# Performance work log

Hardware: AMD Instinct MI355X
Metric: run time of the kernel (lower is better)

The kernel has to match this reference:

```python
import jax, jax.numpy as jnp
import numpy as np

B, S, D, H = 2, 2048, 1024, 16
DH = D // H

def setup_inputs() -> dict:
    key = jax.random.key(0)
    ks = jax.random.split(key, 9)
    s = 1.0 / np.sqrt(D)
    def lin(k):
        kw, kb = jax.random.split(k)
        W = jax.random.uniform(kw, (D, D), jnp.float32, -s, s)
        b = jax.random.uniform(kb, (D,), jnp.float32, -s, s)
        return W, b
    Wq, bq = lin(ks[0]); Wk, bk = lin(ks[1]); Wv, bv = lin(ks[2]); Wo, bo = lin(ks[3])
    x = jax.random.normal(ks[4], (B, S, D), jnp.float32)
    return {"x": x, "Wq": Wq, "bq": bq, "Wk": Wk, "bk": bk,
            "Wv": Wv, "bv": bv, "Wo": Wo, "bo": bo}

def _split_heads(t):
    # [B,S,D] -> [B,H,S,DH]
    return t.reshape(B, S, H, DH).transpose(0, 2, 1, 3)

def reference(x, Wq, bq, Wk, bk, Wv, bv, Wo, bo):
    # torch Linear: y = x @ W.T + b
    q = _split_heads(x @ Wq.T + bq)
    k = _split_heads(x @ Wk.T + bk)
    v = _split_heads(x @ Wv.T + bv)
    scores = jnp.einsum('bhqd,bhkd->bhqk', q, k) / jnp.sqrt(jnp.float32(DH))
    p = jax.nn.softmax(scores, axis=-1)  # dropout is identity in eval
    o = jnp.einsum('bhqk,bhkd->bhqd', p, v)
    o = o.transpose(0, 2, 1, 3).reshape(B, S, D)  # combine heads
    return o @ Wo.T + bo
```

## Files before the change

### kernel.cpp

```cpp
#include <hip/hip_runtime.h>


typedef __bf16 bf16;
typedef bf16 bf16x8 __attribute__((ext_vector_type(8)));
typedef bf16 bf16x4 __attribute__((ext_vector_type(4)));
typedef short s16x4 __attribute__((ext_vector_type(4)));
typedef float f32x4 __attribute__((ext_vector_type(4)));

#define MFMA32(a, b, c) __builtin_amdgcn_mfma_f32_16x16x32_bf16(a, b, c, 0, 0, 0)

#if __has_builtin(__builtin_amdgcn_mfma_f32_16x16x16bf16_1k)
#define HAVE_MFMA16 1
#define MFMA16(a, b, c) __builtin_amdgcn_mfma_f32_16x16x16bf16_1k(a, b, c, 0, 0, 0)
#else
#define HAVE_MFMA16 0
#endif

#define GLL(g, l) __builtin_amdgcn_global_load_lds(                              \
    (const __attribute__((address_space(1))) void*)(const void*)(g),             \
    (__attribute__((address_space(3))) void*)(void*)(l), 16, 0, 0)

union pk4 { bf16x4 h; s16x4 s; unsigned int d[2]; };

__global__ __launch_bounds__(256)
void cvt_bf16(const float* __restrict__ x,  const float* __restrict__ Wq,
              const float* __restrict__ Wk, const float* __restrict__ Wv,
              const float* __restrict__ Wo,
              bf16* __restrict__ xb, bf16* __restrict__ wqb, bf16* __restrict__ wkb,
              bf16* __restrict__ wvb, bf16* __restrict__ wob)
{
    const int idx = blockIdx.x * 256 + threadIdx.x;
    const float* src; bf16* dst; int off;
    if (idx < 1048576) { src = x; dst = xb; off = idx; }
    else {
        const int r = idx - 1048576;
        const int seg = r >> 18;
        off = r & 262143;
        src = (seg == 0) ? Wq : (seg == 1) ? Wk : (seg == 2) ? Wv : Wo;
        dst = (seg == 0) ? wqb : (seg == 1) ? wkb : (seg == 2) ? wvb : wob;
    }
    const float4 v = ((const float4*)src)[off];
    bf16x4 o = {(bf16)v.x, (bf16)v.y, (bf16)v.z, (bf16)v.w};
    *(bf16x4*)(dst + (size_t)off * 4) = o;
}

__global__ __launch_bounds__(256)
void qkv_gemm(const bf16* __restrict__ xb,
              const bf16* __restrict__ wqb, const float* __restrict__ bq,
              const bf16* __restrict__ wkb, const float* __restrict__ bk,
              const bf16* __restrict__ wvb, const float* __restrict__ bv,
              bf16* __restrict__ q_ws, bf16* __restrict__ k_ws, bf16* __restrict__ v_ws)
{
    const int z = blockIdx.z;
    const bf16*  W    = (z == 0) ? wqb : (z == 1) ? wkb : wvb;
    const float* bias = (z == 0) ? bq  : (z == 1) ? bk  : bv;

    __shared__ bf16 As[128][32];
    __shared__ bf16 Bs[128][32];
    __shared__ bf16 Vt[64][132];

    const int m0 = blockIdx.x * 128;
    const int n0 = blockIdx.y * 128;
    const int t    = threadIdx.x;
    const int wave = t >> 6;
    const int lane = t & 63;
    const int lr   = lane & 15;
    const int quad = lane >> 4;
    const int wm = (wave & 1) * 64;
    const int wn = (wave >> 1) * 64;

    const int srow = wave * 32 + (lane >> 2);
    const int scol = (lane & 3) * 8;
    const bf16* ga0 = xb + (size_t)(m0 + srow) * 1024 + scol;
    const bf16* ga1 = xb + (size_t)(m0 + srow + 16) * 1024 + scol;
    const bf16* gb0 = W  + (size_t)(n0 + srow) * 1024 + scol;
    const bf16* gb1 = W  + (size_t)(n0 + srow + 16) * 1024 + scol;
    bf16* la0 = &As[srow][scol];
    bf16* la1 = &As[srow + 16][scol];
    bf16* lb0 = &Bs[srow][scol];
    bf16* lb1 = &Bs[srow + 16][scol];

    f32x4 acc[4][4] = {};

    for (int k0 = 0; k0 < 1024; k0 += 32) {
        GLL(ga0 + k0, la0);
        GLL(ga1 + k0, la1);
        GLL(gb0 + k0, lb0);
        GLL(gb1 + k0, lb1);
        __syncthreads();

        bf16x8 af[4], bfr[4];
        #pragma unroll
        for (int i = 0; i < 4; i++) af[i]  = *(const bf16x8*)&As[wm + i*16 + lr][quad*8];
        #pragma unroll
        for (int j = 0; j < 4; j++) bfr[j] = *(const bf16x8*)&Bs[wn + j*16 + lr][quad*8];
        #pragma unroll
        for (int i = 0; i < 4; i++)
            #pragma unroll
            for (int j = 0; j < 4; j++)
                acc[i][j] = MFMA32(af[i], bfr[j], acc[i][j]);
        __syncthreads();
    }

    if (z < 2) {
        bf16* dstb = (z == 0) ? q_ws : k_ws;
        const float sc = (z == 0) ? 0.125f : 1.0f;
        #pragma unroll
        for (int j = 0; j < 4; j++) {
            const int col = n0 + wn + j * 16 + lr;
            const float bb = bias[col];
            const int h  = col >> 6;
            const int dh = col & 63;
            #pragma unroll
            for (int i = 0; i < 4; i++)
                #pragma unroll
                for (int r = 0; r < 4; r++) {
                    const int row = m0 + wm + i * 16 + quad * 4 + r;
                    const int bi = row >> 11, si = row & 2047;
                    dstb[(((size_t)bi * 16 + h) * 2048 + si) * 64 + dh] =
                        (bf16)((acc[i][j][r] + bb) * sc);
                }
        }
    } else {
        const int bi = m0 >> 11, si0 = m0 & 2047;
        #pragma unroll
        for (int ph = 0; ph < 2; ph++) {
            if ((wave >> 1) == ph) {
                #pragma unroll
                for (int j = 0; j < 4; j++) {
                    const float bb = bias[n0 + ph * 64 + j * 16 + lr];
                    #pragma unroll
                    for (int i = 0; i < 4; i++)
                        #pragma unroll
                        for (int r = 0; r < 4; r++)
                            Vt[j * 16 + lr][wm + i * 16 + quad * 4 + r] =
                                (bf16)(acc[i][j][r] + bb);
                }
            }
            __syncthreads();
            const int c  = t >> 2;
            const int sc_ = (t & 3) * 32;
            const int col = n0 + ph * 64 + c;
            const int h = col >> 6, dh = col & 63;
            bf16* dst = v_ws + (((size_t)bi * 16 + h) * 64 + dh) * 2048 + si0 + sc_;
            #pragma unroll
            for (int e = 0; e < 4; e++)
                *(bf16x8*)(dst + e * 8) = *(const bf16x8*)&Vt[c][sc_ + e * 8];
            __syncthreads();
        }
    }
}

__global__ __launch_bounds__(256, 4)
void attn(const bf16* __restrict__ q_ws, const bf16* __restrict__ k_ws,
          const bf16* __restrict__ v_ws, bf16* __restrict__ o_ws)
{
    const int qt = blockIdx.x;
    const int bh = blockIdx.y;
    const int b_ = bh >> 4, h = bh & 15;

    const bf16* qbase = q_ws + (size_t)bh * 2048 * 64;
    const bf16* kbase = k_ws + (size_t)bh * 2048 * 64;
    const bf16* vbase = v_ws + (size_t)bh * 64 * 2048;

    __shared__ bf16 Ks[128][72];
    __shared__ bf16 Vs[64][136];

    const int t    = threadIdx.x;
    const int wave = t >> 6;
    const int lane = t & 63;
    const int lr   = lane & 15;
    const int quad = lane >> 4;

    bf16x8 aq[2];
    #pragma unroll
    for (int kc = 0; kc < 2; kc++)
        aq[kc] = *(const bf16x8*)(qbase +
            (size_t)(qt*64 + wave*16 + lr) * 64 + kc*32 + quad*8);

    float m_i = -1e30f, l_i = 0.f;
    f32x4 o_accT[4] = {};
    const float C = 1.44269504f;

    for (int kt = 0; kt < 16; kt++) {
        __syncthreads();
        #pragma unroll
        for (int u = 0; u < 4; u++) {
            const int c = t + u * 256;
            *(bf16x8*)&Ks[c >> 3][(c & 7) * 8] =
                *(const bf16x8*)(kbase + (size_t)kt * 128 * 64 + c * 8);
            const int d = c >> 4, off = (c & 15) * 8;
            *(bf16x8*)&Vs[d][off] =
                *(const bf16x8*)(vbase + (size_t)d * 2048 + kt*128 + off);
        }
        __syncthreads();

        f32x4 sacc[8];
        #pragma unroll
        for (int j = 0; j < 8; j++) {
            bf16x8 kf0 = *(const bf16x8*)&Ks[j*16 + lr][quad*8];
            bf16x8 kf1 = *(const bf16x8*)&Ks[j*16 + lr][32 + quad*8];
            f32x4 a = {0.f, 0.f, 0.f, 0.f};
            a = MFMA32(kf0, aq[0], a);
            a = MFMA32(kf1, aq[1], a);
            sacc[j] = a;
        }

        float m = -1e30f;
        #pragma unroll
        for (int j = 0; j < 8; j++)
            #pragma unroll
            for (int r = 0; r < 4; r++) m = fmaxf(m, sacc[j][r]);
        m = fmaxf(m, __shfl_xor(m, 16));
        m = fmaxf(m, __shfl_xor(m, 32));
        const float nm = fmaxf(m_i, m);
        const float al = exp2f((m_i - nm) * C);
        m_i = nm;
        const float nmc = nm * C;
        float rs = 0.f;
        #pragma unroll
        for (int j = 0; j < 8; j++)
            #pragma unroll
            for (int r = 0; r < 4; r++) {
                const float p = exp2f(fmaf(sacc[j][r], C, -nmc));
                sacc[j][r] = p;
                rs += p;
            }
        #pragma unroll
        for (int n = 0; n < 4; n++)
            #pragma unroll
            for (int r = 0; r < 4; r++) o_accT[n][r] *= al;
        rs += __shfl_xor(rs, 16);
        rs += __shfl_xor(rs, 32);
        l_i = l_i * al + rs;

#if HAVE_MFMA16
        #pragma unroll
        for (int j = 0; j < 8; j++) {
            pk4 pf;
            pf.h = bf16x4{(bf16)sacc[j][0], (bf16)sacc[j][1],
                          (bf16)sacc[j][2], (bf16)sacc[j][3]};
            #pragma unroll
            for (int fb = 0; fb < 4; fb++) {
                pk4 vf;
                *(unsigned long long*)vf.d =
                    *(const unsigned long long*)&Vs[fb*16 + lr][j*16 + quad*4];
                o_accT[fb] = MFMA16(vf.s, pf.s, o_accT[fb]);
            }
        }
#else
        unsigned int p0[8], p1[8];
        #pragma unroll
        for (int j = 0; j < 8; j++) {
            pk4 pf;
            pf.h = bf16x4{(bf16)sacc[j][0], (bf16)sacc[j][1],
                          (bf16)sacc[j][2], (bf16)sacc[j][3]};
            p0[j] = pf.d[0]; p1[j] = pf.d[1];
        }
        const int srcA = lr + 16 * ((2 * quad) & 3);
        const int srcB = lr + 16 * ((2 * quad + 1) & 3);
        const bool hi = (quad >> 1) != 0;
        #pragma unroll
        for (int c = 0; c < 4; c++) {
            unsigned int a0 = __shfl(p0[2*c], srcA), a1 = __shfl(p0[2*c+1], srcA);
            unsigned int b0 = __shfl(p1[2*c], srcA), b1 = __shfl(p1[2*c+1], srcA);
            unsigned int c0 = __shfl(p0[2*c], srcB), c1 = __shfl(p0[2*c+1], srcB);
            unsigned int d0 = __shfl(p1[2*c], srcB), d1 = __shfl(p1[2*c+1], srcB);
            unsigned int fr[4];
            fr[0] = hi ? a1 : a0;
            fr[1] = hi ? b1 : b0;
            fr[2] = hi ? c1 : c0;
            fr[3] = hi ? d1 : d0;
            bf16x8 pf8 = *(bf16x8*)fr;
            #pragma unroll
            for (int fb = 0; fb < 4; fb++) {
                bf16x8 vf8 = *(const bf16x8*)&Vs[fb*16 + lr][c*32 + quad*8];
                o_accT[fb] = MFMA32(vf8, pf8, o_accT[fb]);
            }
        }
#endif
    }

    const float inv = 1.0f / l_i;
    const int s = qt*64 + wave*16 + lr;
    #pragma unroll
    for (int fb = 0; fb < 4; fb++) {
        bf16x4 ov = {(bf16)(o_accT[fb][0] * inv), (bf16)(o_accT[fb][1] * inv),
                     (bf16)(o_accT[fb][2] * inv), (bf16)(o_accT[fb][3] * inv)};
        *(bf16x4*)(o_ws + ((size_t)b_ * 2048 + s) * 1024 + h*64 + fb*16 + quad*4) = ov;
    }
}

__global__ __launch_bounds__(256)
void out_gemm(const bf16* __restrict__ o_ws,
              const bf16* __restrict__ wob, const float* __restrict__ bo,
              float* __restrict__ out)
{
    __shared__ bf16 As[128][32];
    __shared__ bf16 Bs[128][32];

    const int m0 = blockIdx.x * 128;
    const int n0 = blockIdx.y * 128;
    const int t    = threadIdx.x;
    const int wave = t >> 6;
    const int lane = t & 63;
    const int lr   = lane & 15;
    const int quad = lane >> 4;
    const int wm = (wave & 1) * 64;
    const int wn = (wave >> 1) * 64;

    const int srow = wave * 32 + (lane >> 2);
    const int scol = (lane & 3) * 8;
    const bf16* ga0 = o_ws + (size_t)(m0 + srow) * 1024 + scol;
    const bf16* ga1 = o_ws + (size_t)(m0 + srow + 16) * 1024 + scol;
    const bf16* gb0 = wob  + (size_t)(n0 + srow) * 1024 + scol;
    const bf16* gb1 = wob  + (size_t)(n0 + srow + 16) * 1024 + scol;
    bf16* la0 = &As[srow][scol];
    bf16* la1 = &As[srow + 16][scol];
    bf16* lb0 = &Bs[srow][scol];
    bf16* lb1 = &Bs[srow + 16][scol];

    f32x4 acc[4][4] = {};

    for (int k0 = 0; k0 < 1024; k0 += 32) {
        GLL(ga0 + k0, la0);
        GLL(ga1 + k0, la1);
        GLL(gb0 + k0, lb0);
        GLL(gb1 + k0, lb1);
        __syncthreads();

        bf16x8 af[4], bfr[4];
        #pragma unroll
        for (int i = 0; i < 4; i++) af[i]  = *(const bf16x8*)&As[wm + i*16 + lr][quad*8];
        #pragma unroll
        for (int j = 0; j < 4; j++) bfr[j] = *(const bf16x8*)&Bs[wn + j*16 + lr][quad*8];
        #pragma unroll
        for (int i = 0; i < 4; i++)
            #pragma unroll
            for (int j = 0; j < 4; j++)
                acc[i][j] = MFMA32(af[i], bfr[j], acc[i][j]);
        __syncthreads();
    }

    #pragma unroll
    for (int j = 0; j < 4; j++) {
        const int col = n0 + wn + j * 16 + lr;
        const float bb = bo[col];
        #pragma unroll
        for (int i = 0; i < 4; i++)
            #pragma unroll
            for (int r = 0; r < 4; r++) {
                const int row = m0 + wm + i * 16 + quad * 4 + r;
                out[(size_t)row * 1024 + col] = acc[i][j][r] + bb;
            }
    }
}

extern "C" void kernel_launch(void* const* d_in, const int* in_sizes, int n_in,
                              void* d_out, int out_size, void* d_ws, size_t ws_size,
                              hipStream_t stream) {
    (void)in_sizes; (void)n_in; (void)out_size; (void)ws_size;
    const float* x  = (const float*)d_in[0];
    const float* Wq = (const float*)d_in[1];
    const float* bq = (const float*)d_in[2];
    const float* Wk = (const float*)d_in[3];
    const float* bk = (const float*)d_in[4];
    const float* Wv = (const float*)d_in[5];
    const float* bv = (const float*)d_in[6];
    const float* Wo = (const float*)d_in[7];
    const float* bo = (const float*)d_in[8];
    float* out = (float*)d_out;

    char* ws = (char*)d_ws;
    const size_t MB = 1024 * 1024;
    bf16* xb   = (bf16*)(ws);
    bf16* wqb  = (bf16*)(ws + 8 * MB);
    bf16* wkb  = (bf16*)(ws + 10 * MB);
    bf16* wvb  = (bf16*)(ws + 12 * MB);
    bf16* wob  = (bf16*)(ws + 14 * MB);
    bf16* q_ws = (bf16*)(ws + 16 * MB);
    bf16* k_ws = (bf16*)(ws + 24 * MB);
    bf16* v_ws = (bf16*)(ws + 32 * MB);
    bf16* o_ws = (bf16*)(ws + 40 * MB);

    hipLaunchKernelGGL(cvt_bf16, dim3(8192), dim3(256), 0, stream,
                       x, Wq, Wk, Wv, Wo, xb, wqb, wkb, wvb, wob);
    hipLaunchKernelGGL(qkv_gemm, dim3(32, 8, 3), dim3(256), 0, stream,
                       xb, wqb, bq, wkb, bk, wvb, bv, q_ws, k_ws, v_ws);
    hipLaunchKernelGGL(attn, dim3(32, 32), dim3(256), 0, stream,
                       q_ws, k_ws, v_ws, o_ws);
    hipLaunchKernelGGL(out_gemm, dim3(32, 8), dim3(256), 0, stream,
                       o_ws, wob, bo, out);
}
```

Measured before the change: 243.8 us.

## Stage GEMM and attention epilogues through LDS, prefetch K/V tiles in registers

Q/K epilogues in qkv_gemm, the attention output, and out_gemm output now go through an LDS staging tile before leaving the kernel. This turns scattered 2-byte and 4-byte scalar global stores into contiguous 16-byte vector stores. The attention kernel also prefetches the next K/V tile into registers while the current tile is being computed, which overlaps global load latency with MFMA work. out_gemm shrinks its M tile to 64 and doubles the grid to fill more CUs. The cost is extra LDS traffic, more barriers, and higher register pressure in attention.

```diff
diff --git a/kernel.cpp b/kernel.cpp
--- a/kernel.cpp
+++ b/kernel.cpp
@@ -57,7 +57,9 @@
 
     __shared__ bf16 As[128][32];
     __shared__ bf16 Bs[128][32];
-    __shared__ bf16 Vt[64][132];
+    __shared__ char ebuf[17408];
+    bf16 (*Et)[68]  = (bf16(*)[68])ebuf;
+    bf16 (*Vt)[132] = (bf16(*)[132])ebuf;
 
     const int m0 = blockIdx.x * 128;
     const int n0 = blockIdx.y * 128;
@@ -102,27 +104,35 @@
         __syncthreads();
     }
 
+    const int bi = m0 >> 11, si0 = m0 & 2047;
     if (z < 2) {
-        bf16* dstb = (z == 0) ? q_ws : k_ws;
+        bf16* hw = (z == 0) ? q_ws : k_ws;
         const float sc = (z == 0) ? 0.125f : 1.0f;
         #pragma unroll
-        for (int j = 0; j < 4; j++) {
-            const int col = n0 + wn + j * 16 + lr;
-            const float bb = bias[col];
-            const int h  = col >> 6;
-            const int dh = col & 63;
-            #pragma unroll
-            for (int i = 0; i < 4; i++)
+        for (int ph = 0; ph < 2; ph++) {
+            if ((wave >> 1) == ph) {
                 #pragma unroll
-                for (int r = 0; r < 4; r++) {
-                    const int row = m0 + wm + i * 16 + quad * 4 + r;
-                    const int bi = row >> 11, si = row & 2047;
-                    dstb[(((size_t)bi * 16 + h) * 2048 + si) * 64 + dh] =
-                        (bf16)((acc[i][j][r] + bb) * sc);
+                for (int j = 0; j < 4; j++) {
+                    const float bb = bias[n0 + ph * 64 + j * 16 + lr];
+                    #pragma unroll
+                    for (int i = 0; i < 4; i++)
+                        #pragma unroll
+                        for (int r = 0; r < 4; r++)
+                            Et[wm + i*16 + quad*4 + r][j*16 + lr] =
+                                (bf16)((acc[i][j][r] + bb) * sc);
                 }
+            }
+            __syncthreads();
+            const int hh = (n0 >> 6) + ph;
+            bf16* dst = hw + (((size_t)bi * 16 + hh) * 2048 + si0) * 64;
+            const int row = t >> 1, cc = (t & 1) * 32;
+            #pragma unroll
+            for (int e = 0; e < 4; e++)
+                *(bf16x8*)(dst + (size_t)row * 64 + cc + e * 8) =
+                    *(const bf16x8*)&Et[row][cc + e * 8];
+            __syncthreads();
         }
     } else {
-        const int bi = m0 >> 11, si0 = m0 & 2047;
         #pragma unroll
         for (int ph = 0; ph < 2; ph++) {
             if ((wave >> 1) == ph) {
@@ -182,18 +192,32 @@
     f32x4 o_accT[4] = {};
     const float C = 1.44269504f;
 
+    bf16x8 kreg[4], vreg[4];
+    #pragma unroll
+    for (int u = 0; u < 4; u++) {
+        const int c = t + u * 256;
+        kreg[u] = *(const bf16x8*)(kbase + (size_t)c * 8);
+        vreg[u] = *(const bf16x8*)(vbase + (size_t)(c >> 4) * 2048 + (c & 15) * 8);
+    }
+
     for (int kt = 0; kt < 16; kt++) {
         __syncthreads();
         #pragma unroll
         for (int u = 0; u < 4; u++) {
             const int c = t + u * 256;
-            *(bf16x8*)&Ks[c >> 3][(c & 7) * 8] =
-                *(const bf16x8*)(kbase + (size_t)kt * 128 * 64 + c * 8);
-            const int d = c >> 4, off = (c & 15) * 8;
-            *(bf16x8*)&Vs[d][off] =
-                *(const bf16x8*)(vbase + (size_t)d * 2048 + kt*128 + off);
-        }
-        __syncthreads();
+            *(bf16x8*)&Ks[c >> 3][(c & 7) * 8] = kreg[u];
+            *(bf16x8*)&Vs[c >> 4][(c & 15) * 8] = vreg[u];
+        }
+        __syncthreads();
+        if (kt < 15) {
+            #pragma unroll
+            for (int u = 0; u < 4; u++) {
+                const int c = t + u * 256;
+                kreg[u] = *(const bf16x8*)(kbase + (size_t)(kt+1) * 8192 + c * 8);
+                vreg[u] = *(const bf16x8*)(vbase + (size_t)(c >> 4) * 2048
+                                           + (kt+1) * 128 + (c & 15) * 8);
+            }
+        }
 
         f32x4 sacc[8];
         #pragma unroll
@@ -281,14 +305,20 @@
 #endif
     }
 
+    __syncthreads();
+    bf16 (*OsE)[68] = (bf16(*)[68])&Ks[0][0];
     const float inv = 1.0f / l_i;
-    const int s = qt*64 + wave*16 + lr;
+    const int sil = wave * 16 + lr;
     #pragma unroll
-    for (int fb = 0; fb < 4; fb++) {
-        bf16x4 ov = {(bf16)(o_accT[fb][0] * inv), (bf16)(o_accT[fb][1] * inv),
-                     (bf16)(o_accT[fb][2] * inv), (bf16)(o_accT[fb][3] * inv)};
-        *(bf16x4*)(o_ws + ((size_t)b_ * 2048 + s) * 1024 + h*64 + fb*16 + quad*4) = ov;
-    }
+    for (int fb = 0; fb < 4; fb++)
+        #pragma unroll
+        for (int r = 0; r < 4; r++)
+            OsE[sil][fb*16 + quad*4 + r] = (bf16)(o_accT[fb][r] * inv);
+    __syncthreads();
+    const int row = t >> 2, seg = (t & 3) * 16;
+    bf16* dst = o_ws + ((size_t)b_ * 2048 + qt*64 + row) * 1024 + h*64 + seg;
+    *(bf16x8*)(dst)     = *(const bf16x8*)&OsE[row][seg];
+    *(bf16x8*)(dst + 8) = *(const bf16x8*)&OsE[row][seg + 8];
 }
 
 __global__ __launch_bounds__(256)
@@ -296,46 +326,45 @@
               const bf16* __restrict__ wob, const float* __restrict__ bo,
               float* __restrict__ out)
 {
-    __shared__ bf16 As[128][32];
+    __shared__ bf16 As[64][32];
     __shared__ bf16 Bs[128][32];
-
-    const int m0 = blockIdx.x * 128;
+    __shared__ float Ot[64][68];
+
+    const int m0 = blockIdx.x * 64;
     const int n0 = blockIdx.y * 128;
     const int t    = threadIdx.x;
     const int wave = t >> 6;
     const int lane = t & 63;
     const int lr   = lane & 15;
     const int quad = lane >> 4;
-    const int wm = (wave & 1) * 64;
+    const int wm = (wave & 1) * 32;
     const int wn = (wave >> 1) * 64;
 
-    const int srow = wave * 32 + (lane >> 2);
-    const int scol = (lane & 3) * 8;
-    const bf16* ga0 = o_ws + (size_t)(m0 + srow) * 1024 + scol;
-    const bf16* ga1 = o_ws + (size_t)(m0 + srow + 16) * 1024 + scol;
-    const bf16* gb0 = wob  + (size_t)(n0 + srow) * 1024 + scol;
-    const bf16* gb1 = wob  + (size_t)(n0 + srow + 16) * 1024 + scol;
-    bf16* la0 = &As[srow][scol];
-    bf16* la1 = &As[srow + 16][scol];
-    bf16* lb0 = &Bs[srow][scol];
-    bf16* lb1 = &Bs[srow + 16][scol];
-
-    f32x4 acc[4][4] = {};
+    const int srowA = wave * 16 + (lane >> 2);
+    const int srowB = wave * 32 + (lane >> 2);
+    const int scol  = (lane & 3) * 8;
+    const bf16* gaA = o_ws + (size_t)(m0 + srowA) * 1024 + scol;
+    const bf16* gb0 = wob  + (size_t)(n0 + srowB) * 1024 + scol;
+    const bf16* gb1 = wob  + (size_t)(n0 + srowB + 16) * 1024 + scol;
+    bf16* laA = &As[srowA][scol];
+    bf16* lb0 = &Bs[srowB][scol];
+    bf16* lb1 = &Bs[srowB + 16][scol];
+
+    f32x4 acc[2][4] = {};
 
     for (int k0 = 0; k0 < 1024; k0 += 32) {
-        GLL(ga0 + k0, la0);
-        GLL(ga1 + k0, la1);
+        GLL(gaA + k0, laA);
         GLL(gb0 + k0, lb0);
         GLL(gb1 + k0, lb1);
         __syncthreads();
 
-        bf16x8 af[4], bfr[4];
-        #pragma unroll
-        for (int i = 0; i < 4; i++) af[i]  = *(const bf16x8*)&As[wm + i*16 + lr][quad*8];
+        bf16x8 af[2], bfr[4];
+        #pragma unroll
+        for (int i = 0; i < 2; i++) af[i]  = *(const bf16x8*)&As[wm + i*16 + lr][quad*8];
         #pragma unroll
         for (int j = 0; j < 4; j++) bfr[j] = *(const bf16x8*)&Bs[wn + j*16 + lr][quad*8];
         #pragma unroll
-        for (int i = 0; i < 4; i++)
+        for (int i = 0; i < 2; i++)
             #pragma unroll
             for (int j = 0; j < 4; j++)
                 acc[i][j] = MFMA32(af[i], bfr[j], acc[i][j]);
@@ -343,16 +372,25 @@
     }
 
     #pragma unroll
-    for (int j = 0; j < 4; j++) {
-        const int col = n0 + wn + j * 16 + lr;
-        const float bb = bo[col];
-        #pragma unroll
-        for (int i = 0; i < 4; i++)
-            #pragma unroll
-            for (int r = 0; r < 4; r++) {
-                const int row = m0 + wm + i * 16 + quad * 4 + r;
-                out[(size_t)row * 1024 + col] = acc[i][j][r] + bb;
-            }
+    for (int ph = 0; ph < 2; ph++) {
+        if ((wave >> 1) == ph) {
+            #pragma unroll
+            for (int j = 0; j < 4; j++) {
+                const float bb = bo[n0 + ph * 64 + j * 16 + lr];
+                #pragma unroll
+                for (int i = 0; i < 2; i++)
+                    #pragma unroll
+                    for (int r = 0; r < 4; r++)
+                        Ot[wm + i*16 + quad*4 + r][j*16 + lr] = acc[i][j][r] + bb;
+            }
+        }
+        __syncthreads();
+        const int row = t >> 2, seg = (t & 3) * 16;
+        float* dst = out + (size_t)(m0 + row) * 1024 + n0 + ph * 64 + seg;
+        #pragma unroll
+        for (int e = 0; e < 4; e++)
+            *(float4*)(dst + e * 4) = *(const float4*)&Ot[row][seg + e * 4];
+        __syncthreads();
     }
 }
 
@@ -389,6 +427,6 @@
                        xb, wqb, bq, wkb, bk, wvb, bv, q_ws, k_ws, v_ws);
     hipLaunchKernelGGL(attn, dim3(32, 32), dim3(256), 0, stream,
                        q_ws, k_ws, v_ws, o_ws);
-    hipLaunchKernelGGL(out_gemm, dim3(32, 8), dim3(256), 0, stream,
+    hipLaunchKernelGGL(out_gemm, dim3(64, 8), dim3(256), 0, stream,
                        o_ws, wob, bo, out);
 }
```

After: 240.1 us. About the same (-1.5%).
